# Kernel tuning notes

Hardware: AMD Instinct MI355X
Metric: run time of the kernel (lower is better)

## Reference

```python
import jax, jax.numpy as jnp
import numpy as np

B, S, H, L = 8, 512, 768, 8192


def setup_inputs() -> dict:
    key = jax.random.key(0)
    k1, k2, k3, k4 = jax.random.split(key, 4)
    inputs = jax.random.normal(k1, (B, S, H), dtype=jnp.float32)
    masks = jax.random.randint(k2, (B, 1, S), 0, 2).astype(jnp.bool_)
    # guarantee at least one valid position per row so softmax is finite
    masks = masks.at[:, :, 0].set(True)
    # xavier-normal label embedding [L, H] (frozen param in original)
    std_emb = float(np.sqrt(2.0 / (L + H)))
    label_embedding = jax.random.normal(k3, (L, H), dtype=jnp.float32) * std_emb
    # xavier-uniform key weight [H, H] (nn.Linear stores W as [out, in])
    lim = float(np.sqrt(6.0 / (H + H)))
    W_key = jax.random.uniform(k4, (H, H), dtype=jnp.float32, minval=-lim, maxval=lim)
    return {"inputs": inputs, "masks": masks, "label_embedding": label_embedding, "W_key": W_key}


def reference(inputs, masks, label_embedding, W_key):
    # key projection: inputs @ W_key^T  -> [B, S, H]
    attn_key = jnp.einsum("bsh,kh->bsk", inputs, W_key)
    # scores: label_emb @ key^T -> [B, L, S] (no 1/sqrt(d) scaling, per original)
    scores = jnp.einsum("lh,bsh->bls", label_embedding, attn_key)
    scores = jnp.where(masks, scores, -jnp.inf)  # masks [B,1,S] broadcasts over L
    attn = jax.nn.softmax(scores, axis=-1)
    # weighted sum of raw inputs -> [B, L, H]
    return jnp.einsum("bls,bsh->blh", attn, inputs)
```

## Files before the change

kernel.cpp:

```cpp
#include <hip/hip_runtime.h>
#include <hip/hip_bf16.h>
#include <math.h>

#define NB 8
#define NS 512
#define NH 768
#define NL 8192

typedef __attribute__((ext_vector_type(8))) __bf16 bf16x8;
typedef __attribute__((ext_vector_type(4))) float f32x4;

static __device__ __forceinline__ f32x4 mfma_bf16(bf16x8 a, bf16x8 b, f32x4 c) {
  return __builtin_amdgcn_mfma_f32_16x16x32_bf16(a, b, c, 0, 0, 0);
}

static __device__ __forceinline__ void llds16(const void* g, void* l) {
  __builtin_amdgcn_global_load_lds(
      (const __attribute__((address_space(1))) unsigned int*)g,
      (__attribute__((address_space(3))) unsigned int*)l, 16, 0, 0);
}

static __device__ __forceinline__ bf16x8 load_cvt8(const float* __restrict__ p) {
  f32x4 u0 = *(const f32x4*)p;
  f32x4 u1 = *(const f32x4*)(p + 4);
  bf16x8 r;
  r[0] = (__bf16)u0[0]; r[1] = (__bf16)u0[1]; r[2] = (__bf16)u0[2]; r[3] = (__bf16)u0[3];
  r[4] = (__bf16)u1[0]; r[5] = (__bf16)u1[1]; r[6] = (__bf16)u1[2]; r[7] = (__bf16)u1[3];
  return r;
}

__global__ void detect_mask_kernel(const unsigned char* __restrict__ m,
                                   int* __restrict__ flag) {
  __shared__ int s_i8, s_f32;
  if (threadIdx.x == 0) { s_i8 = 0; s_f32 = 0; }
  __syncthreads();
  const unsigned int* md = (const unsigned int*)m;
  int li8 = 0, lf = 0;
  for (int i = threadIdx.x; i < 1024; i += blockDim.x) {
    unsigned int d = md[i];
    if (d == 0x3F800000u) lf = 1;
    if (d & 0xFFFFFF00u) li8 = 1;
  }
  if (li8) atomicOr(&s_i8, 1);
  if (lf) atomicOr(&s_f32, 1);
  __syncthreads();
  if (threadIdx.x == 0) *flag = s_f32 ? 2 : (s_i8 ? 1 : 0);
}

__global__ void expand_mask_kernel(const void* __restrict__ m,
                                   const int* __restrict__ flag,
                                   float* __restrict__ mbias) {
  int i = blockIdx.x * blockDim.x + threadIdx.x;
  int f = *flag;
  int v;
  if (f == 1)      v = (((const unsigned char*)m)[i] != 0);
  else if (f == 2) v = (((const float*)m)[i] != 0.0f);
  else             v = (((const int*)m)[i] != 0);
  mbias[i] = v ? 0.0f : -INFINITY;
}

__global__ __launch_bounds__(256) void cast_kernel(const float* __restrict__ src,
                                                   __bf16* __restrict__ dst) {
  size_t idx = ((size_t)blockIdx.x * 256 + threadIdx.x) * 8;
  bf16x8 v = load_cvt8(src + idx);
  *(bf16x8*)(dst + idx) = v;
}

__global__ __launch_bounds__(256) void transpose_kernel(const float* __restrict__ X,
                                                        __bf16* __restrict__ XT) {
  __shared__ float t[64][65];
  const int b = blockIdx.z, s0 = blockIdx.y * 64, h0 = blockIdx.x * 64;
  const int j = threadIdx.x & 63, i0 = threadIdx.x >> 6;
  const float* Xb = X + ((size_t)b * NS + s0) * NH + h0;
#pragma unroll
  for (int i = i0; i < 64; i += 4) t[i][j] = Xb[(size_t)i * NH + j];
  __syncthreads();
  __bf16* XTb = XT + ((size_t)b * NH + h0) * NS + s0;
  const int si = threadIdx.x & 63, j0 = threadIdx.x >> 6;
#pragma unroll
  for (int jj = j0; jj < 64; jj += 4)
    XTb[(size_t)jj * NS + si] = (__bf16)t[si][jj];
}

__global__ __launch_bounds__(256, 3) void proj_staged_kernel(
    const __bf16* __restrict__ Xbf, const __bf16* __restrict__ Wbf,
    __bf16* __restrict__ Kout) {
  const int tid = threadIdx.x, lane = tid & 63, wid = tid >> 6;
  const int c = lane & 15, g = lane >> 4;
  const int wm = wid >> 1, wn = wid & 1;
  const int m0 = blockIdx.x * 128;
  const int n0 = blockIdx.y * 128;
  __shared__ __align__(16) unsigned char smem[2][16384];

  f32x4 acc[4][4];
#pragma unroll
  for (int i = 0; i < 4; ++i)
#pragma unroll
    for (int j = 0; j < 4; ++j) acc[i][j] = (f32x4){0.f, 0.f, 0.f, 0.f};

  auto stage = [&](int buf, int k0) {
#pragma unroll
    for (int it = 0; it < 2; ++it) {
      int ch = it * 4 + wid;
      int idx = ch * 64 + lane;
      int row = idx >> 2, slot = idx & 3;
      llds16(Xbf + (size_t)(m0 + row) * NH + k0 + slot * 8, &smem[buf][ch * 1024]);
      llds16(Wbf + (size_t)(n0 + row) * NH + k0 + slot * 8, &smem[buf][8192 + ch * 1024]);
    }
  };

  stage(0, 0);
  __syncthreads();
  int cur = 0;
  for (int t = 0; t < 24; ++t) {
    if (t < 23) stage(cur ^ 1, (t + 1) * 32);
    const unsigned char* A = smem[cur];
    const unsigned char* B = smem[cur] + 8192;
    bf16x8 af[4], bfr[4];
#pragma unroll
    for (int fm = 0; fm < 4; ++fm)
      af[fm] = *(const bf16x8*)(A + (wm * 64 + fm * 16 + c) * 64 + g * 16);
#pragma unroll
    for (int fn = 0; fn < 4; ++fn)
      bfr[fn] = *(const bf16x8*)(B + (wn * 64 + fn * 16 + c) * 64 + g * 16);
#pragma unroll
    for (int fm = 0; fm < 4; ++fm)
#pragma unroll
      for (int fn = 0; fn < 4; ++fn)
        acc[fm][fn] = mfma_bf16(af[fm], bfr[fn], acc[fm][fn]);
    __syncthreads();
    cur ^= 1;
  }
#pragma unroll
  for (int fm = 0; fm < 4; ++fm)
#pragma unroll
    for (int r = 0; r < 4; ++r) {
      int row = m0 + wm * 64 + fm * 16 + g * 4 + r;
#pragma unroll
      for (int fn = 0; fn < 4; ++fn)
        Kout[(size_t)row * NH + n0 + wn * 64 + fn * 16 + c] = (__bf16)acc[fm][fn][r];
    }
}

__global__ __launch_bounds__(512, 2) void scores_kernel(
    const __bf16* __restrict__ Ebf,
    const __bf16* __restrict__ Kbf,
    const float* __restrict__ mbias,
    __bf16* __restrict__ Pws) {
  const int tid = threadIdx.x, lane = tid & 63, wid = tid >> 6;
  const int c = lane & 15, g = lane >> 4;
  const int wm = wid >> 2, wn = wid & 3;
  const int b = blockIdx.y;
  const int R0 = blockIdx.x * 128;
  __shared__ __align__(16) unsigned char smem[2][40960];
  const __bf16* Kb0 = Kbf + (size_t)b * NS * NH;

  f32x4 acc[4][8];
#pragma unroll
  for (int i = 0; i < 4; ++i)
#pragma unroll
    for (int j = 0; j < 8; ++j) acc[i][j] = (f32x4){0.f, 0.f, 0.f, 0.f};

  auto stage = [&](int buf, int k0) {
    {
      int idx = wid * 64 + lane;
      int row = idx >> 2, slot = idx & 3;
      llds16(Ebf + (size_t)(R0 + row) * NH + k0 + slot * 8, &smem[buf][wid * 1024]);
    }
#pragma unroll
    for (int it = 0; it < 4; ++it) {
      int bc = it * 8 + wid;
      int idx = bc * 64 + lane;
      int row = idx >> 2, slot = idx & 3;
      llds16(Kb0 + (size_t)row * NH + k0 + slot * 8, &smem[buf][8192 + bc * 1024]);
    }
  };

  stage(0, 0);
  __syncthreads();
  int cur = 0;
  for (int t = 0; t < 24; ++t) {
    if (t < 23) stage(cur ^ 1, (t + 1) * 32);
    const unsigned char* A = smem[cur];
    const unsigned char* B = smem[cur] + 8192;
    bf16x8 af[4], bfr[8];
#pragma unroll
    for (int fm = 0; fm < 4; ++fm)
      af[fm] = *(const bf16x8*)(A + (wm * 64 + fm * 16 + c) * 64 + g * 16);
#pragma unroll
    for (int fn = 0; fn < 8; ++fn)
      bfr[fn] = *(const bf16x8*)(B + (wn * 128 + fn * 16 + c) * 64 + g * 16);
#pragma unroll
    for (int fm = 0; fm < 4; ++fm)
#pragma unroll
      for (int fn = 0; fn < 8; ++fn)
        acc[fm][fn] = mfma_bf16(af[fm], bfr[fn], acc[fm][fn]);
    __syncthreads();
    cur ^= 1;
  }

  float* red = (float*)smem;
  float bias[8];
#pragma unroll
  for (int fn = 0; fn < 8; ++fn) bias[fn] = mbias[b * NS + wn * 128 + fn * 16 + c];

  float rmax[4][4];
#pragma unroll
  for (int fm = 0; fm < 4; ++fm)
#pragma unroll
    for (int r = 0; r < 4; ++r) {
      float v = -INFINITY;
#pragma unroll
      for (int fn = 0; fn < 8; ++fn) v = fmaxf(v, acc[fm][fn][r] + bias[fn]);
      v = fmaxf(v, __shfl_xor(v, 1));
      v = fmaxf(v, __shfl_xor(v, 2));
      v = fmaxf(v, __shfl_xor(v, 4));
      v = fmaxf(v, __shfl_xor(v, 8));
      if (c == 0) red[wn * 128 + wm * 64 + fm * 16 + g * 4 + r] = v;
    }
  __syncthreads();
#pragma unroll
  for (int fm = 0; fm < 4; ++fm)
#pragma unroll
    for (int r = 0; r < 4; ++r) {
      int row = wm * 64 + fm * 16 + g * 4 + r;
      rmax[fm][r] = fmaxf(fmaxf(red[row], red[128 + row]),
                          fmaxf(red[256 + row], red[384 + row]));
    }
  __syncthreads();

  float sums[4][4];
#pragma unroll
  for (int fm = 0; fm < 4; ++fm)
#pragma unroll
    for (int r = 0; r < 4; ++r) {
      float s = 0.f;
#pragma unroll
      for (int fn = 0; fn < 8; ++fn) {
        float p = __expf(acc[fm][fn][r] + bias[fn] - rmax[fm][r]);
        acc[fm][fn][r] = p;
        s += p;
      }
      s += __shfl_xor(s, 1);
      s += __shfl_xor(s, 2);
      s += __shfl_xor(s, 4);
      s += __shfl_xor(s, 8);
      if (c == 0) red[wn * 128 + wm * 64 + fm * 16 + g * 4 + r] = s;
      sums[fm][r] = 0.f;
      (void)sums;
    }
  __syncthreads();

  __bf16* Pb = Pws + ((size_t)b * NL + R0) * NS;
#pragma unroll
  for (int fm = 0; fm < 4; ++fm)
#pragma unroll
    for (int r = 0; r < 4; ++r) {
      int row = wm * 64 + fm * 16 + g * 4 + r;
      float inv = 1.0f / (red[row] + red[128 + row] + red[256 + row] + red[384 + row]);
#pragma unroll
      for (int fn = 0; fn < 8; ++fn)
        Pb[(size_t)row * NS + wn * 128 + fn * 16 + c] = (__bf16)(acc[fm][fn][r] * inv);
    }
}

__global__ __launch_bounds__(256, 3) void pv_kernel(
    const __bf16* __restrict__ Pws,
    const __bf16* __restrict__ XTbf,
    float* __restrict__ Out) {
  const int tid = threadIdx.x, lane = tid & 63, wid = tid >> 6;
  const int c = lane & 15, g = lane >> 4;
  const int wm = wid >> 1, wn = wid & 1;
  const int b = blockIdx.z;
  const size_t rowbase = (size_t)b * NL + (size_t)blockIdx.x * 128;
  const int h0 = blockIdx.y * 128;
  __shared__ __align__(16) unsigned char smem[2][16384];
  const __bf16* Xb0 = XTbf + (size_t)b * NH * NS;

  f32x4 acc[4][4];
#pragma unroll
  for (int i = 0; i < 4; ++i)
#pragma unroll
    for (int j = 0; j < 4; ++j) acc[i][j] = (f32x4){0.f, 0.f, 0.f, 0.f};

  auto stage = [&](int buf, int k0) {
#pragma unroll
    for (int it = 0; it < 2; ++it) {
      int ch = it * 4 + wid;
      int idx = ch * 64 + lane;
      int row = idx >> 2, slot = idx & 3;
      llds16(Pws + (rowbase + row) * NS + k0 + slot * 8, &smem[buf][ch * 1024]);
      llds16(Xb0 + (size_t)(h0 + row) * NS + k0 + slot * 8, &smem[buf][8192 + ch * 1024]);
    }
  };

  stage(0, 0);
  __syncthreads();
  int cur = 0;
  for (int t = 0; t < 16; ++t) {
    if (t < 15) stage(cur ^ 1, (t + 1) * 32);
    const unsigned char* A = smem[cur];
    const unsigned char* B = smem[cur] + 8192;
    bf16x8 af[4], bfr[4];
#pragma unroll
    for (int fm = 0; fm < 4; ++fm)
      af[fm] = *(const bf16x8*)(A + (wm * 64 + fm * 16 + c) * 64 + g * 16);
#pragma unroll
    for (int fn = 0; fn < 4; ++fn)
      bfr[fn] = *(const bf16x8*)(B + (wn * 64 + fn * 16 + c) * 64 + g * 16);
#pragma unroll
    for (int fm = 0; fm < 4; ++fm)
#pragma unroll
      for (int fn = 0; fn < 4; ++fn)
        acc[fm][fn] = mfma_bf16(af[fm], bfr[fn], acc[fm][fn]);
    __syncthreads();
    cur ^= 1;
  }
  float* Ob = Out + rowbase * NH;
#pragma unroll
  for (int fm = 0; fm < 4; ++fm)
#pragma unroll
    for (int r = 0; r < 4; ++r) {
      int row = wm * 64 + fm * 16 + g * 4 + r;
#pragma unroll
      for (int fn = 0; fn < 4; ++fn)
        Ob[(size_t)row * NH + h0 + wn * 64 + fn * 16 + c] = acc[fm][fn][r];
    }
}

__global__ __launch_bounds__(256) void proj_kernel(const float* __restrict__ X,
                                                   const float* __restrict__ W,
                                                   __bf16* __restrict__ Kout) {
  const int tid = threadIdx.x;
  const int lane = tid & 63, wid = tid >> 6;
  const int c = lane & 15, g = lane >> 4;
  const int wm = wid >> 1, wn = wid & 1;
  const int m0 = blockIdx.x * 64 + wm * 32;
  const int n0 = blockIdx.y * 64 + wn * 32;
  f32x4 acc[2][2] = {};
  const float* Xp = X + (size_t)(m0 + c) * NH + g * 8;
  const float* Wp = W + (size_t)(n0 + c) * NH + g * 8;
  for (int k = 0; k < NH; k += 32) {
    bf16x8 a0 = load_cvt8(Xp + k);
    bf16x8 a1 = load_cvt8(Xp + 16 * NH + k);
    bf16x8 b0 = load_cvt8(Wp + k);
    bf16x8 b1 = load_cvt8(Wp + 16 * NH + k);
    acc[0][0] = mfma_bf16(a0, b0, acc[0][0]);
    acc[0][1] = mfma_bf16(a0, b1, acc[0][1]);
    acc[1][0] = mfma_bf16(a1, b0, acc[1][0]);
    acc[1][1] = mfma_bf16(a1, b1, acc[1][1]);
  }
#pragma unroll
  for (int fm = 0; fm < 2; ++fm)
#pragma unroll
    for (int fn = 0; fn < 2; ++fn)
#pragma unroll
      for (int r = 0; r < 4; ++r) {
        int row = m0 + fm * 16 + g * 4 + r;
        int col = n0 + fn * 16 + c;
        Kout[(size_t)row * NH + col] = (__bf16)acc[fm][fn][r];
      }
}

__global__ __launch_bounds__(512) void label_attn_kernel(
    const __bf16* __restrict__ Ebf, const __bf16* __restrict__ Kbf,
    const __bf16* __restrict__ XTbf, const float* __restrict__ mbias,
    float* __restrict__ Out) {
  const int tid = threadIdx.x;
  const int lane = tid & 63, wid = tid >> 6;
  const int c = lane & 15, g = lane >> 4;
  const int wm = wid >> 2, wn = wid & 3;
  const int b = blockIdx.y;
  const int R0 = blockIdx.x * 64;
  __shared__ alignas(16) __bf16 Plds[64 * 512];
  __shared__ float redM[4][64];
  __shared__ float redS[4][64];
  f32x4 acc[2][8];
#pragma unroll
  for (int i = 0; i < 2; ++i)
#pragma unroll
    for (int j = 0; j < 8; ++j) acc[i][j] = (f32x4){0.f, 0.f, 0.f, 0.f};
  const __bf16* Ea = Ebf + (size_t)(R0 + wm * 32 + c) * NH + g * 8;
  const __bf16* Kb = Kbf + ((size_t)b * NS + wn * 128 + c) * NH + g * 8;
  float bias[8];
#pragma unroll
  for (int fn = 0; fn < 8; ++fn) bias[fn] = mbias[b * NS + wn * 128 + fn * 16 + c];
  for (int k = 0; k < NH; k += 32) {
    bf16x8 a0 = *(const bf16x8*)(Ea + k);
    bf16x8 a1 = *(const bf16x8*)(Ea + 16 * NH + k);
#pragma unroll
    for (int fn = 0; fn < 8; ++fn) {
      bf16x8 bb = *(const bf16x8*)(Kb + (size_t)fn * 16 * NH + k);
      acc[0][fn] = mfma_bf16(a0, bb, acc[0][fn]);
      acc[1][fn] = mfma_bf16(a1, bb, acc[1][fn]);
    }
  }
  float pmax[2][4];
#pragma unroll
  for (int fm = 0; fm < 2; ++fm)
#pragma unroll
    for (int r = 0; r < 4; ++r) {
      float v = -INFINITY;
#pragma unroll
      for (int fn = 0; fn < 8; ++fn) v = fmaxf(v, acc[fm][fn][r] + bias[fn]);
#pragma unroll
      for (int off = 1; off < 16; off <<= 1) v = fmaxf(v, __shfl_xor(v, off));
      pmax[fm][r] = v;
    }
  if (c == 0) {
#pragma unroll
    for (int fm = 0; fm < 2; ++fm)
#pragma unroll
      for (int r = 0; r < 4; ++r)
        redM[wn][wm * 32 + fm * 16 + g * 4 + r] = pmax[fm][r];
  }
  __syncthreads();
  float rmax[2][4];
#pragma unroll
  for (int fm = 0; fm < 2; ++fm)
#pragma unroll
    for (int r = 0; r < 4; ++r) {
      int row = wm * 32 + fm * 16 + g * 4 + r;
      rmax[fm][r] = fmaxf(fmaxf(redM[0][row], redM[1][row]),
                          fmaxf(redM[2][row], redM[3][row]));
    }
  float psum[2][4] = {{0.f, 0.f, 0.f, 0.f}, {0.f, 0.f, 0.f, 0.f}};
#pragma unroll
  for (int fm = 0; fm < 2; ++fm)
#pragma unroll
    for (int fn = 0; fn < 8; ++fn) {
      int col = wn * 128 + fn * 16 + c;
#pragma unroll
      for (int r = 0; r < 4; ++r) {
        int row = wm * 32 + fm * 16 + g * 4 + r;
        float p = __expf(acc[fm][fn][r] + bias[fn] - rmax[fm][r]);
        psum[fm][r] += p;
        Plds[row * 512 + (col ^ ((row & 7) << 3))] = (__bf16)p;
      }
    }
#pragma unroll
  for (int fm = 0; fm < 2; ++fm)
#pragma unroll
    for (int r = 0; r < 4; ++r) {
      float v = psum[fm][r];
#pragma unroll
      for (int off = 1; off < 16; off <<= 1) v += __shfl_xor(v, off);
      psum[fm][r] = v;
    }
  if (c == 0) {
#pragma unroll
    for (int fm = 0; fm < 2; ++fm)
#pragma unroll
      for (int r = 0; r < 4; ++r)
        redS[wn][wm * 32 + fm * 16 + g * 4 + r] = psum[fm][r];
  }
  __syncthreads();
  float inv[2][4];
#pragma unroll
  for (int fm = 0; fm < 2; ++fm)
#pragma unroll
    for (int r = 0; r < 4; ++r) {
      int row = wm * 32 + fm * 16 + g * 4 + r;
      float s = redS[0][row] + redS[1][row] + redS[2][row] + redS[3][row];
      inv[fm][r] = 1.0f / s;
    }
  f32x4 acc2[2][12];
#pragma unroll
  for (int i = 0; i < 2; ++i)
#pragma unroll
    for (int j = 0; j < 12; ++j) acc2[i][j] = (f32x4){0.f, 0.f, 0.f, 0.f};
  const __bf16* XTb = XTbf + ((size_t)b * NH + wn * 192 + c) * NS + g * 8;
  const int r0 = wm * 32 + c;
  const int r1 = r0 + 16;
  for (int ks = 0; ks < NS; ks += 32) {
    int kk = ks + g * 8;
    bf16x8 a0 = *(const bf16x8*)&Plds[r0 * 512 + (kk ^ ((r0 & 7) << 3))];
    bf16x8 a1 = *(const bf16x8*)&Plds[r1 * 512 + (kk ^ ((r1 & 7) << 3))];
#pragma unroll
    for (int fn = 0; fn < 12; ++fn) {
      bf16x8 bb = *(const bf16x8*)(XTb + (size_t)fn * 16 * NS + ks);
      acc2[0][fn] = mfma_bf16(a0, bb, acc2[0][fn]);
      acc2[1][fn] = mfma_bf16(a1, bb, acc2[1][fn]);
    }
  }
  float* Ob = Out + ((size_t)b * NL + R0) * NH;
#pragma unroll
  for (int fm = 0; fm < 2; ++fm)
#pragma unroll
    for (int r = 0; r < 4; ++r) {
      int row = wm * 32 + fm * 16 + g * 4 + r;
      float sc = inv[fm][r];
#pragma unroll
      for (int fn = 0; fn < 12; ++fn) {
        int h = wn * 192 + fn * 16 + c;
        Ob[(size_t)row * NH + h] = acc2[fm][fn][r] * sc;
      }
    }
}

extern "C" void kernel_launch(void* const* d_in, const int* in_sizes, int n_in,
                              void* d_out, int out_size, void* d_ws, size_t ws_size,
                              hipStream_t stream) {
  const float* X = (const float*)d_in[0];
  const void* masks = d_in[1];
  const float* E = (const float*)d_in[2];
  const float* W = (const float*)d_in[3];
  float* Out = (float*)d_out;

  char* ws = (char*)d_ws;
  const size_t NEED = 99762432;

  if (ws_size >= NEED) {
    __bf16* Pws  = (__bf16*)ws;
    __bf16* Ebf  = (__bf16*)(ws + 67108864);
    __bf16* Kbf  = (__bf16*)(ws + 79691776);
    __bf16* XTbf = (__bf16*)(ws + 85983232);
    __bf16* Xbf  = (__bf16*)(ws + 92274688);
    __bf16* Wbf  = (__bf16*)(ws + 98566144);
    float* mbias = (float*)(ws + 99745792);
    int* flag    = (int*)(ws + 99762176);

    detect_mask_kernel<<<1, 256, 0, stream>>>((const unsigned char*)masks, flag);
    expand_mask_kernel<<<16, 256, 0, stream>>>(masks, flag, mbias);
    cast_kernel<<<1536, 256, 0, stream>>>(X, Xbf);
    cast_kernel<<<288, 256, 0, stream>>>(W, Wbf);
    cast_kernel<<<3072, 256, 0, stream>>>(E, Ebf);
    transpose_kernel<<<dim3(12, 8, 8), 256, 0, stream>>>(X, XTbf);
    proj_staged_kernel<<<dim3(32, 6), 256, 0, stream>>>(Xbf, Wbf, Kbf);
    scores_kernel<<<dim3(64, 8), 512, 0, stream>>>(Ebf, Kbf, mbias, Pws);
    pv_kernel<<<dim3(64, 6, 8), 256, 0, stream>>>(Pws, XTbf, Out);
  } else {
    __bf16* Kbf  = (__bf16*)ws;
    __bf16* XTbf = (__bf16*)(ws + 6291456);
    __bf16* Ebf  = (__bf16*)(ws + 12582912);
    float* mbias = (float*)(ws + 25165824);
    int* flag    = (int*)(ws + 25182208);

    detect_mask_kernel<<<1, 256, 0, stream>>>((const unsigned char*)masks, flag);
    expand_mask_kernel<<<16, 256, 0, stream>>>(masks, flag, mbias);
    proj_kernel<<<dim3(64, 12), 256, 0, stream>>>(X, W, Kbf);
    transpose_kernel<<<dim3(12, 8, 8), 256, 0, stream>>>(X, XTbf);
    cast_kernel<<<3072, 256, 0, stream>>>(E, Ebf);
    label_attn_kernel<<<dim3(128, 8), 512, 0, stream>>>(Ebf, Kbf, XTbf, mbias, Out);
  }
}
```

Measured before the change: 389.0 us.

## Fuse scores, softmax and PV into one kernel keeping probabilities in LDS

Replaces the separate scores and PV kernels, which passed a 64MB bf16 probability matrix through global memory, with a fused kernel. It computes 64 label rows of scores against all 512 keys, does the masked softmax in registers and LDS, and multiplies the swizzled LDS probabilities by the transposed inputs. It also merges the mask detect and expand kernels and the three cast kernels into single launches, and uses a smaller 64x64 projection tile to raise the block count. The fused kernel uses a large LDS footprint at one block per CU, and it recomputes nothing but gives up the occupancy of the split kernels.

After: 474.6 us. 22.0% more time.

```diff
diff --git a/kernel.cpp b/kernel.cpp
--- a/kernel.cpp
+++ b/kernel.cpp
@@ -27,6 +27,301 @@
   r[0] = (__bf16)u0[0]; r[1] = (__bf16)u0[1]; r[2] = (__bf16)u0[2]; r[3] = (__bf16)u0[3];
   r[4] = (__bf16)u1[0]; r[5] = (__bf16)u1[1]; r[6] = (__bf16)u1[2]; r[7] = (__bf16)u1[3];
   return r;
+}
+
+__global__ void mask_kernel(const unsigned char* __restrict__ m,
+                            float* __restrict__ mbias) {
+  __shared__ int s_i8, s_f32;
+  if (threadIdx.x == 0) { s_i8 = 0; s_f32 = 0; }
+  __syncthreads();
+  const unsigned int* md = (const unsigned int*)m;
+  int li8 = 0, lf = 0;
+  for (int i = threadIdx.x; i < 1024; i += blockDim.x) {
+    unsigned int d = md[i];
+    if (d == 0x3F800000u) lf = 1;
+    if (d & 0xFFFFFF00u) li8 = 1;
+  }
+  if (li8) atomicOr(&s_i8, 1);
+  if (lf) atomicOr(&s_f32, 1);
+  __syncthreads();
+  int f = s_f32 ? 2 : (s_i8 ? 1 : 0);
+  for (int i = threadIdx.x; i < NB * NS; i += blockDim.x) {
+    int v;
+    if (f == 1)      v = (((const unsigned char*)m)[i] != 0);
+    else if (f == 2) v = (((const float*)m)[i] != 0.0f);
+    else             v = (((const int*)m)[i] != 0);
+    mbias[i] = v ? 0.0f : -INFINITY;
+  }
+}
+
+#define XT8 393216
+#define WT8 466944
+#define ET8 1253376
+__global__ __launch_bounds__(256) void cast_all_kernel(
+    const float* __restrict__ X, const float* __restrict__ W,
+    const float* __restrict__ E, __bf16* __restrict__ dstbase) {
+  size_t t8 = (size_t)blockIdx.x * 256 + threadIdx.x;
+  const float* src;
+  size_t off;
+  if (t8 < XT8)      { src = X; off = t8 * 8; }
+  else if (t8 < WT8) { src = W; off = (t8 - XT8) * 8; }
+  else               { src = E; off = (t8 - WT8) * 8; }
+  bf16x8 v = load_cvt8(src + off);
+  *(bf16x8*)(dstbase + t8 * 8) = v;
+}
+
+__global__ __launch_bounds__(256) void transpose_kernel(const float* __restrict__ X,
+                                                        __bf16* __restrict__ XT) {
+  __shared__ float t[64][65];
+  const int b = blockIdx.z, s0 = blockIdx.y * 64, h0 = blockIdx.x * 64;
+  const int j = threadIdx.x & 63, i0 = threadIdx.x >> 6;
+#pragma unroll
+  for (int i = i0; i < 64; i += 4) t[i][j] = X[((size_t)b * NS + s0 + i) * NH + h0 + j];
+  __syncthreads();
+  __bf16* XTb = XT + ((size_t)b * NH + h0) * NS + s0;
+  const int si = threadIdx.x & 63, j0 = threadIdx.x >> 6;
+#pragma unroll
+  for (int jj = j0; jj < 64; jj += 4)
+    XTb[(size_t)jj * NS + si] = (__bf16)t[si][jj];
+}
+
+__global__ __launch_bounds__(256, 4) void proj64_kernel(
+    const __bf16* __restrict__ Xbf, const __bf16* __restrict__ Wbf,
+    __bf16* __restrict__ Kout) {
+  const int tid = threadIdx.x, lane = tid & 63, wid = tid >> 6;
+  const int c = lane & 15, g = lane >> 4;
+  const int wm = wid >> 1, wn = wid & 1;
+  const int m0 = blockIdx.x * 64, n0 = blockIdx.y * 64;
+  __shared__ __align__(16) unsigned char Ast[2][4096];
+  __shared__ __align__(16) unsigned char Bst[2][4096];
+
+  f32x4 acc[2][2];
+#pragma unroll
+  for (int i = 0; i < 2; ++i)
+#pragma unroll
+    for (int j = 0; j < 2; ++j) acc[i][j] = (f32x4){0.f, 0.f, 0.f, 0.f};
+
+  auto stage = [&](int buf, int k0) {
+    int idx = wid * 64 + lane;
+    int row = idx >> 2, slot = idx & 3;
+    llds16(Xbf + (size_t)(m0 + row) * NH + k0 + slot * 8, &Ast[buf][wid * 1024]);
+    llds16(Wbf + (size_t)(n0 + row) * NH + k0 + slot * 8, &Bst[buf][wid * 1024]);
+  };
+
+  stage(0, 0);
+  __syncthreads();
+  int cur = 0;
+  for (int t = 0; t < 24; ++t) {
+    if (t < 23) stage(cur ^ 1, (t + 1) * 32);
+    bf16x8 af[2], bfr[2];
+#pragma unroll
+    for (int fm = 0; fm < 2; ++fm)
+      af[fm] = *(const bf16x8*)&Ast[cur][(wm * 32 + fm * 16 + c) * 64 + g * 16];
+#pragma unroll
+    for (int fn = 0; fn < 2; ++fn)
+      bfr[fn] = *(const bf16x8*)&Bst[cur][(wn * 32 + fn * 16 + c) * 64 + g * 16];
+#pragma unroll
+    for (int fm = 0; fm < 2; ++fm)
+#pragma unroll
+      for (int fn = 0; fn < 2; ++fn)
+        acc[fm][fn] = mfma_bf16(af[fm], bfr[fn], acc[fm][fn]);
+    __syncthreads();
+    cur ^= 1;
+  }
+#pragma unroll
+  for (int fm = 0; fm < 2; ++fm)
+#pragma unroll
+    for (int r = 0; r < 4; ++r) {
+      int row = m0 + wm * 32 + fm * 16 + g * 4 + r;
+#pragma unroll
+      for (int fn = 0; fn < 2; ++fn)
+        Kout[(size_t)row * NH + n0 + wn * 32 + fn * 16 + c] = (__bf16)acc[fm][fn][r];
+    }
+}
+
+__global__ __launch_bounds__(512, 1) void fused_attn_kernel(
+    const __bf16* __restrict__ Ebf,
+    const __bf16* __restrict__ Kbf,
+    const __bf16* __restrict__ XTbf,
+    const float* __restrict__ mbias,
+    float* __restrict__ Out) {
+  const int tid = threadIdx.x, lane = tid & 63, wid = tid >> 6;
+  const int c = lane & 15, g = lane >> 4;
+  const int b = blockIdx.y;
+  const int R0 = blockIdx.x * 64;
+
+  __shared__ __align__(16) __bf16 Plds[64 * 512];
+  __shared__ __align__(16) unsigned char Ast[2][4096];
+  __shared__ __align__(16) unsigned char Bst[2][32768];
+  __shared__ float red[8][64];
+
+  const __bf16* Kb0 = Kbf + (size_t)b * NS * NH;
+
+  f32x4 acc[4][4];
+#pragma unroll
+  for (int i = 0; i < 4; ++i)
+#pragma unroll
+    for (int j = 0; j < 4; ++j) acc[i][j] = (f32x4){0.f, 0.f, 0.f, 0.f};
+
+  auto stage1 = [&](int buf, int k0) {
+    if (wid < 4) {
+      int idx = wid * 64 + lane;
+      int row = idx >> 2, slot = idx & 3;
+      llds16(Ebf + (size_t)(R0 + row) * NH + k0 + slot * 8, &Ast[buf][wid * 1024]);
+    }
+#pragma unroll
+    for (int it = 0; it < 4; ++it) {
+      int ch = it * 8 + wid;
+      int idx = ch * 64 + lane;
+      int srow = idx >> 2, slot = idx & 3;
+      llds16(Kb0 + (size_t)srow * NH + k0 + slot * 8, &Bst[buf][ch * 1024]);
+    }
+  };
+
+  stage1(0, 0);
+  __syncthreads();
+  int cur = 0;
+  for (int t = 0; t < 24; ++t) {
+    if (t < 23) stage1(cur ^ 1, (t + 1) * 32);
+    bf16x8 af[4], bfr[4];
+#pragma unroll
+    for (int fm = 0; fm < 4; ++fm)
+      af[fm] = *(const bf16x8*)&Ast[cur][(fm * 16 + c) * 64 + g * 16];
+#pragma unroll
+    for (int fn = 0; fn < 4; ++fn)
+      bfr[fn] = *(const bf16x8*)&Bst[cur][(wid * 64 + fn * 16 + c) * 64 + g * 16];
+#pragma unroll
+    for (int fm = 0; fm < 4; ++fm)
+#pragma unroll
+      for (int fn = 0; fn < 4; ++fn)
+        acc[fm][fn] = mfma_bf16(af[fm], bfr[fn], acc[fm][fn]);
+    __syncthreads();
+    cur ^= 1;
+  }
+
+  float bias[4];
+#pragma unroll
+  for (int fn = 0; fn < 4; ++fn) bias[fn] = mbias[b * NS + wid * 64 + fn * 16 + c];
+
+#pragma unroll
+  for (int fm = 0; fm < 4; ++fm)
+#pragma unroll
+    for (int r = 0; r < 4; ++r) {
+      float v = -INFINITY;
+#pragma unroll
+      for (int fn = 0; fn < 4; ++fn) v = fmaxf(v, acc[fm][fn][r] + bias[fn]);
+      v = fmaxf(v, __shfl_xor(v, 1));
+      v = fmaxf(v, __shfl_xor(v, 2));
+      v = fmaxf(v, __shfl_xor(v, 4));
+      v = fmaxf(v, __shfl_xor(v, 8));
+      if (c == 0) red[wid][fm * 16 + g * 4 + r] = v;
+    }
+  __syncthreads();
+  float rmax[4][4];
+#pragma unroll
+  for (int fm = 0; fm < 4; ++fm)
+#pragma unroll
+    for (int r = 0; r < 4; ++r) {
+      int l = fm * 16 + g * 4 + r;
+      float v = red[0][l];
+#pragma unroll
+      for (int w = 1; w < 8; ++w) v = fmaxf(v, red[w][l]);
+      rmax[fm][r] = v;
+    }
+  __syncthreads();
+
+#pragma unroll
+  for (int fm = 0; fm < 4; ++fm)
+#pragma unroll
+    for (int r = 0; r < 4; ++r) {
+      float s = 0.f;
+#pragma unroll
+      for (int fn = 0; fn < 4; ++fn) {
+        float p = __expf(acc[fm][fn][r] + bias[fn] - rmax[fm][r]);
+        acc[fm][fn][r] = p;
+        s += p;
+      }
+      s += __shfl_xor(s, 1);
+      s += __shfl_xor(s, 2);
+      s += __shfl_xor(s, 4);
+      s += __shfl_xor(s, 8);
+      if (c == 0) red[wid][fm * 16 + g * 4 + r] = s;
+    }
+  __syncthreads();
+
+#pragma unroll
+  for (int fm = 0; fm < 4; ++fm)
+#pragma unroll
+    for (int r = 0; r < 4; ++r) {
+      int l = fm * 16 + g * 4 + r;
+      float s = red[0][l];
+#pragma unroll
+      for (int w = 1; w < 8; ++w) s += red[w][l];
+      float inv = 1.0f / s;
+#pragma unroll
+      for (int fn = 0; fn < 4; ++fn) {
+        int col = wid * 64 + fn * 16 + c;
+        Plds[l * 512 + (col ^ ((l & 7) << 3))] = (__bf16)(acc[fm][fn][r] * inv);
+      }
+    }
+  __syncthreads();
+
+  const __bf16* XTb0 = XTbf + (size_t)b * NH * NS;
+  float* Ob = Out + ((size_t)b * NL + R0) * NH;
+
+  for (int nh = 0; nh < 2; ++nh) {
+    const int h0 = nh * 384;
+    f32x4 acc2[4][3];
+#pragma unroll
+    for (int i = 0; i < 4; ++i)
+#pragma unroll
+      for (int j = 0; j < 3; ++j) acc2[i][j] = (f32x4){0.f, 0.f, 0.f, 0.f};
+
+    auto stage2 = [&](int buf, int ks) {
+#pragma unroll
+      for (int j = 0; j < 3; ++j) {
+        int ch = wid * 3 + j;
+        int idx = ch * 64 + lane;
+        int hrow = idx >> 2, slot = idx & 3;
+        llds16(XTb0 + (size_t)(h0 + hrow) * NS + ks + slot * 8, &Bst[buf][ch * 1024]);
+      }
+    };
+
+    stage2(0, 0);
+    __syncthreads();
+    cur = 0;
+    for (int t = 0; t < 16; ++t) {
+      if (t < 15) stage2(cur ^ 1, (t + 1) * 32);
+      int kk = t * 32 + g * 8;
+      bf16x8 af[4], bfr[3];
+#pragma unroll
+      for (int fm = 0; fm < 4; ++fm) {
+        int l = fm * 16 + c;
+        af[fm] = *(const bf16x8*)&Plds[l * 512 + (kk ^ ((l & 7) << 3))];
+      }
+#pragma unroll
+      for (int fn = 0; fn < 3; ++fn)
+        bfr[fn] = *(const bf16x8*)&Bst[cur][(wid * 48 + fn * 16 + c) * 64 + g * 16];
+#pragma unroll
+      for (int fm = 0; fm < 4; ++fm)
+#pragma unroll
+        for (int fn = 0; fn < 3; ++fn)
+          acc2[fm][fn] = mfma_bf16(af[fm], bfr[fn], acc2[fm][fn]);
+      __syncthreads();
+      cur ^= 1;
+    }
+#pragma unroll
+    for (int fm = 0; fm < 4; ++fm)
+#pragma unroll
+      for (int r = 0; r < 4; ++r) {
+        int l = fm * 16 + g * 4 + r;
+#pragma unroll
+        for (int fn = 0; fn < 3; ++fn) {
+          int h = h0 + wid * 48 + fn * 16 + c;
+          Ob[(size_t)l * NH + h] = acc2[fm][fn][r];
+        }
+      }
+  }
 }
 
 __global__ void detect_mask_kernel(const unsigned char* __restrict__ m,
@@ -64,268 +359,6 @@
   size_t idx = ((size_t)blockIdx.x * 256 + threadIdx.x) * 8;
   bf16x8 v = load_cvt8(src + idx);
   *(bf16x8*)(dst + idx) = v;
-}
-
-__global__ __launch_bounds__(256) void transpose_kernel(const float* __restrict__ X,
-                                                        __bf16* __restrict__ XT) {
-  __shared__ float t[64][65];
-  const int b = blockIdx.z, s0 = blockIdx.y * 64, h0 = blockIdx.x * 64;
-  const int j = threadIdx.x & 63, i0 = threadIdx.x >> 6;
-  const float* Xb = X + ((size_t)b * NS + s0) * NH + h0;
-#pragma unroll
-  for (int i = i0; i < 64; i += 4) t[i][j] = Xb[(size_t)i * NH + j];
-  __syncthreads();
-  __bf16* XTb = XT + ((size_t)b * NH + h0) * NS + s0;
-  const int si = threadIdx.x & 63, j0 = threadIdx.x >> 6;
-#pragma unroll
-  for (int jj = j0; jj < 64; jj += 4)
-    XTb[(size_t)jj * NS + si] = (__bf16)t[si][jj];
-}
-
-__global__ __launch_bounds__(256, 3) void proj_staged_kernel(
-    const __bf16* __restrict__ Xbf, const __bf16* __restrict__ Wbf,
-    __bf16* __restrict__ Kout) {
-  const int tid = threadIdx.x, lane = tid & 63, wid = tid >> 6;
-  const int c = lane & 15, g = lane >> 4;
-  const int wm = wid >> 1, wn = wid & 1;
-  const int m0 = blockIdx.x * 128;
-  const int n0 = blockIdx.y * 128;
-  __shared__ __align__(16) unsigned char smem[2][16384];
-
-  f32x4 acc[4][4];
-#pragma unroll
-  for (int i = 0; i < 4; ++i)
-#pragma unroll
-    for (int j = 0; j < 4; ++j) acc[i][j] = (f32x4){0.f, 0.f, 0.f, 0.f};
-
-  auto stage = [&](int buf, int k0) {
-#pragma unroll
-    for (int it = 0; it < 2; ++it) {
-      int ch = it * 4 + wid;
-      int idx = ch * 64 + lane;
-      int row = idx >> 2, slot = idx & 3;
-      llds16(Xbf + (size_t)(m0 + row) * NH + k0 + slot * 8, &smem[buf][ch * 1024]);
-      llds16(Wbf + (size_t)(n0 + row) * NH + k0 + slot * 8, &smem[buf][8192 + ch * 1024]);
-    }
-  };
-
-  stage(0, 0);
-  __syncthreads();
-  int cur = 0;
-  for (int t = 0; t < 24; ++t) {
-    if (t < 23) stage(cur ^ 1, (t + 1) * 32);
-    const unsigned char* A = smem[cur];
-    const unsigned char* B = smem[cur] + 8192;
-    bf16x8 af[4], bfr[4];
-#pragma unroll
-    for (int fm = 0; fm < 4; ++fm)
-      af[fm] = *(const bf16x8*)(A + (wm * 64 + fm * 16 + c) * 64 + g * 16);
-#pragma unroll
-    for (int fn = 0; fn < 4; ++fn)
-      bfr[fn] = *(const bf16x8*)(B + (wn * 64 + fn * 16 + c) * 64 + g * 16);
-#pragma unroll
-    for (int fm = 0; fm < 4; ++fm)
-#pragma unroll
-      for (int fn = 0; fn < 4; ++fn)
-        acc[fm][fn] = mfma_bf16(af[fm], bfr[fn], acc[fm][fn]);
-    __syncthreads();
-    cur ^= 1;
-  }
-#pragma unroll
-  for (int fm = 0; fm < 4; ++fm)
-#pragma unroll
-    for (int r = 0; r < 4; ++r) {
-      int row = m0 + wm * 64 + fm * 16 + g * 4 + r;
-#pragma unroll
-      for (int fn = 0; fn < 4; ++fn)
-        Kout[(size_t)row * NH + n0 + wn * 64 + fn * 16 + c] = (__bf16)acc[fm][fn][r];
-    }
-}
-
-__global__ __launch_bounds__(512, 2) void scores_kernel(
-    const __bf16* __restrict__ Ebf,
-    const __bf16* __restrict__ Kbf,
-    const float* __restrict__ mbias,
-    __bf16* __restrict__ Pws) {
-  const int tid = threadIdx.x, lane = tid & 63, wid = tid >> 6;
-  const int c = lane & 15, g = lane >> 4;
-  const int wm = wid >> 2, wn = wid & 3;
-  const int b = blockIdx.y;
-  const int R0 = blockIdx.x * 128;
-  __shared__ __align__(16) unsigned char smem[2][40960];
-  const __bf16* Kb0 = Kbf + (size_t)b * NS * NH;
-
-  f32x4 acc[4][8];
-#pragma unroll
-  for (int i = 0; i < 4; ++i)
-#pragma unroll
-    for (int j = 0; j < 8; ++j) acc[i][j] = (f32x4){0.f, 0.f, 0.f, 0.f};
-
-  auto stage = [&](int buf, int k0) {
-    {
-      int idx = wid * 64 + lane;
-      int row = idx >> 2, slot = idx & 3;
-      llds16(Ebf + (size_t)(R0 + row) * NH + k0 + slot * 8, &smem[buf][wid * 1024]);
-    }
-#pragma unroll
-    for (int it = 0; it < 4; ++it) {
-      int bc = it * 8 + wid;
-      int idx = bc * 64 + lane;
-      int row = idx >> 2, slot = idx & 3;
-      llds16(Kb0 + (size_t)row * NH + k0 + slot * 8, &smem[buf][8192 + bc * 1024]);
-    }
-  };
-
-  stage(0, 0);
-  __syncthreads();
-  int cur = 0;
-  for (int t = 0; t < 24; ++t) {
-    if (t < 23) stage(cur ^ 1, (t + 1) * 32);
-    const unsigned char* A = smem[cur];
-    const unsigned char* B = smem[cur] + 8192;
-    bf16x8 af[4], bfr[8];
-#pragma unroll
-    for (int fm = 0; fm < 4; ++fm)
-      af[fm] = *(const bf16x8*)(A + (wm * 64 + fm * 16 + c) * 64 + g * 16);
-#pragma unroll
-    for (int fn = 0; fn < 8; ++fn)
-      bfr[fn] = *(const bf16x8*)(B + (wn * 128 + fn * 16 + c) * 64 + g * 16);
-#pragma unroll
-    for (int fm = 0; fm < 4; ++fm)
-#pragma unroll
-      for (int fn = 0; fn < 8; ++fn)
-        acc[fm][fn] = mfma_bf16(af[fm], bfr[fn], acc[fm][fn]);
-    __syncthreads();
-    cur ^= 1;
-  }
-
-  float* red = (float*)smem;
-  float bias[8];
-#pragma unroll
-  for (int fn = 0; fn < 8; ++fn) bias[fn] = mbias[b * NS + wn * 128 + fn * 16 + c];
-
-  float rmax[4][4];
-#pragma unroll
-  for (int fm = 0; fm < 4; ++fm)
-#pragma unroll
-    for (int r = 0; r < 4; ++r) {
-      float v = -INFINITY;
-#pragma unroll
-      for (int fn = 0; fn < 8; ++fn) v = fmaxf(v, acc[fm][fn][r] + bias[fn]);
-      v = fmaxf(v, __shfl_xor(v, 1));
-      v = fmaxf(v, __shfl_xor(v, 2));
-      v = fmaxf(v, __shfl_xor(v, 4));
-      v = fmaxf(v, __shfl_xor(v, 8));
-      if (c == 0) red[wn * 128 + wm * 64 + fm * 16 + g * 4 + r] = v;
-    }
-  __syncthreads();
-#pragma unroll
-  for (int fm = 0; fm < 4; ++fm)
-#pragma unroll
-    for (int r = 0; r < 4; ++r) {
-      int row = wm * 64 + fm * 16 + g * 4 + r;
-      rmax[fm][r] = fmaxf(fmaxf(red[row], red[128 + row]),
-                          fmaxf(red[256 + row], red[384 + row]));
-    }
-  __syncthreads();
-
-  float sums[4][4];
-#pragma unroll
-  for (int fm = 0; fm < 4; ++fm)
-#pragma unroll
-    for (int r = 0; r < 4; ++r) {
-      float s = 0.f;
-#pragma unroll
-      for (int fn = 0; fn < 8; ++fn) {
-        float p = __expf(acc[fm][fn][r] + bias[fn] - rmax[fm][r]);
-        acc[fm][fn][r] = p;
-        s += p;
-      }
-      s += __shfl_xor(s, 1);
-      s += __shfl_xor(s, 2);
-      s += __shfl_xor(s, 4);
-      s += __shfl_xor(s, 8);
-      if (c == 0) red[wn * 128 + wm * 64 + fm * 16 + g * 4 + r] = s;
-      sums[fm][r] = 0.f;
-      (void)sums;
-    }
-  __syncthreads();
-
-  __bf16* Pb = Pws + ((size_t)b * NL + R0) * NS;
-#pragma unroll
-  for (int fm = 0; fm < 4; ++fm)
-#pragma unroll
-    for (int r = 0; r < 4; ++r) {
-      int row = wm * 64 + fm * 16 + g * 4 + r;
-      float inv = 1.0f / (red[row] + red[128 + row] + red[256 + row] + red[384 + row]);
-#pragma unroll
-      for (int fn = 0; fn < 8; ++fn)
-        Pb[(size_t)row * NS + wn * 128 + fn * 16 + c] = (__bf16)(acc[fm][fn][r] * inv);
-    }
-}
-
-__global__ __launch_bounds__(256, 3) void pv_kernel(
-    const __bf16* __restrict__ Pws,
-    const __bf16* __restrict__ XTbf,
-    float* __restrict__ Out) {
-  const int tid = threadIdx.x, lane = tid & 63, wid = tid >> 6;
-  const int c = lane & 15, g = lane >> 4;
-  const int wm = wid >> 1, wn = wid & 1;
-  const int b = blockIdx.z;
-  const size_t rowbase = (size_t)b * NL + (size_t)blockIdx.x * 128;
-  const int h0 = blockIdx.y * 128;
-  __shared__ __align__(16) unsigned char smem[2][16384];
-  const __bf16* Xb0 = XTbf + (size_t)b * NH * NS;
-
-  f32x4 acc[4][4];
-#pragma unroll
-  for (int i = 0; i < 4; ++i)
-#pragma unroll
-    for (int j = 0; j < 4; ++j) acc[i][j] = (f32x4){0.f, 0.f, 0.f, 0.f};
-
-  auto stage = [&](int buf, int k0) {
-#pragma unroll
-    for (int it = 0; it < 2; ++it) {
-      int ch = it * 4 + wid;
-      int idx = ch * 64 + lane;
-      int row = idx >> 2, slot = idx & 3;
-      llds16(Pws + (rowbase + row) * NS + k0 + slot * 8, &smem[buf][ch * 1024]);
-      llds16(Xb0 + (size_t)(h0 + row) * NS + k0 + slot * 8, &smem[buf][8192 + ch * 1024]);
-    }
-  };
-
-  stage(0, 0);
-  __syncthreads();
-  int cur = 0;
-  for (int t = 0; t < 16; ++t) {
-    if (t < 15) stage(cur ^ 1, (t + 1) * 32);
-    const unsigned char* A = smem[cur];
-    const unsigned char* B = smem[cur] + 8192;
-    bf16x8 af[4], bfr[4];
-#pragma unroll
-    for (int fm = 0; fm < 4; ++fm)
-      af[fm] = *(const bf16x8*)(A + (wm * 64 + fm * 16 + c) * 64 + g * 16);
-#pragma unroll
-    for (int fn = 0; fn < 4; ++fn)
-      bfr[fn] = *(const bf16x8*)(B + (wn * 64 + fn * 16 + c) * 64 + g * 16);
-#pragma unroll
-    for (int fm = 0; fm < 4; ++fm)
-#pragma unroll
-      for (int fn = 0; fn < 4; ++fn)
-        acc[fm][fn] = mfma_bf16(af[fm], bfr[fn], acc[fm][fn]);
-    __syncthreads();
-    cur ^= 1;
-  }
-  float* Ob = Out + rowbase * NH;
-#pragma unroll
-  for (int fm = 0; fm < 4; ++fm)
-#pragma unroll
-    for (int r = 0; r < 4; ++r) {
-      int row = wm * 64 + fm * 16 + g * 4 + r;
-#pragma unroll
-      for (int fn = 0; fn < 4; ++fn)
-        Ob[(size_t)row * NH + h0 + wn * 64 + fn * 16 + c] = acc[fm][fn][r];
-    }
 }
 
 __global__ __launch_bounds__(256) void proj_kernel(const float* __restrict__ X,
@@ -508,27 +541,21 @@
   float* Out = (float*)d_out;
 
   char* ws = (char*)d_ws;
-  const size_t NEED = 99762432;
+  const size_t NEED = 32653312;
 
   if (ws_size >= NEED) {
-    __bf16* Pws  = (__bf16*)ws;
-    __bf16* Ebf  = (__bf16*)(ws + 67108864);
-    __bf16* Kbf  = (__bf16*)(ws + 79691776);
-    __bf16* XTbf = (__bf16*)(ws + 85983232);
-    __bf16* Xbf  = (__bf16*)(ws + 92274688);
-    __bf16* Wbf  = (__bf16*)(ws + 98566144);
-    float* mbias = (float*)(ws + 99745792);
-    int* flag    = (int*)(ws + 99762176);
-
-    detect_mask_kernel<<<1, 256, 0, stream>>>((const unsigned char*)masks, flag);
-    expand_mask_kernel<<<16, 256, 0, stream>>>(masks, flag, mbias);
-    cast_kernel<<<1536, 256, 0, stream>>>(X, Xbf);
-    cast_kernel<<<288, 256, 0, stream>>>(W, Wbf);
-    cast_kernel<<<3072, 256, 0, stream>>>(E, Ebf);
+    __bf16* Xbf  = (__bf16*)ws;
+    __bf16* Wbf  = (__bf16*)(ws + 6291456);
+    __bf16* Ebf  = (__bf16*)(ws + 7471104);
+    __bf16* Kbf  = (__bf16*)(ws + 20054016);
+    __bf16* XTbf = (__bf16*)(ws + 26345472);
+    float* mbias = (float*)(ws + 32636928);
+
+    mask_kernel<<<1, 256, 0, stream>>>((const unsigned char*)masks, mbias);
+    cast_all_kernel<<<4896, 256, 0, stream>>>(X, W, E, Xbf);
     transpose_kernel<<<dim3(12, 8, 8), 256, 0, stream>>>(X, XTbf);
-    proj_staged_kernel<<<dim3(32, 6), 256, 0, stream>>>(Xbf, Wbf, Kbf);
-    scores_kernel<<<dim3(64, 8), 512, 0, stream>>>(Ebf, Kbf, mbias, Pws);
-    pv_kernel<<<dim3(64, 6, 8), 256, 0, stream>>>(Pws, XTbf, Out);
+    proj64_kernel<<<dim3(64, 12), 256, 0, stream>>>(Xbf, Wbf, Kbf);
+    fused_attn_kernel<<<dim3(128, 8), 512, 0, stream>>>(Ebf, Kbf, XTbf, mbias, Out);
   } else {
     __bf16* Kbf  = (__bf16*)ws;
     __bf16* XTbf = (__bf16*)(ws + 6291456);
```
